# Kernel optimization log

Measured on AMD Instinct MI355X. Metric: run time of the kernel, lower is better.

Reference implementation:

```python
import jax, jax.numpy as jnp
import numpy as np

N_NODES = 100000
N_EDGES = 1600000
IN_DIM, HID, OUT_DIM = 8, 64, 32
LN_EPS = 1e-5


def _layer_norm(x, g, b):
    m = jnp.mean(x, axis=-1, keepdims=True)
    v = jnp.var(x, axis=-1, keepdims=True)
    return g * (x - m) / jnp.sqrt(v + LN_EPS) + b


def _gat(h, W, a, src, dst, n_nodes):
    # Wh: [N, H]
    Wh = h @ W
    # per-edge score: dot(Wh[src], Wh[dst]) * sum(a)  (leaky relu, slope 0.2)
    s = jnp.sum(Wh[src] * Wh[dst], axis=-1)  # [E]
    e = jax.nn.leaky_relu(s * jnp.sum(a), negative_slope=0.2)
    att = jax.nn.softmax(e)  # NOTE: global softmax over ALL edges, as in source
    msg = att[:, None] * Wh[src]  # [E, H]
    h_prime = jax.ops.segment_sum(msg, dst, num_segments=n_nodes)
    return jax.nn.elu(h_prime)


def _stack(x, src, dst, params):
    out = x
    for (W, a, g, b) in params:
        out = _layer_norm(_gat(out, W, a, src, dst, N_NODES), g, b)
    return out


def setup_inputs() -> dict:
    key = jax.random.key(0)
    ks = jax.random.split(key, 24)
    d = {}
    d['x'] = jax.random.normal(ks[0], (N_NODES, IN_DIM), dtype=jnp.float32)
    d['edge_index'] = jax.random.randint(ks[1], (2, N_EDGES), 0, N_NODES, dtype=jnp.int32)
    d['edge_type'] = jax.random.randint(ks[2], (N_EDGES,), 0, 2, dtype=jnp.int32)
    d['temporal_edge_index'] = jax.random.randint(ks[3], (2, N_EDGES), 0, N_NODES, dtype=jnp.int32)

    def xavier(k, shape):
        fan_in, fan_out = shape[0], shape[1]
        lim = float(np.sqrt(6.0 / (fan_in + fan_out)))
        return jax.random.uniform(k, shape, jnp.float32, -lim, lim)

    i = 4
    for pfx in ('s', 't'):
        for li, ind in enumerate((IN_DIM, HID)):
            d[f'{pfx}W{li}'] = xavier(ks[i], (ind, HID)); i += 1
            d[f'{pfx}a{li}'] = xavier(ks[i], (2 * HID, 1)); i += 1
            d[f'{pfx}g{li}'] = jnp.ones((HID,), jnp.float32)
            d[f'{pfx}b{li}'] = jnp.zeros((HID,), jnp.float32)
    d['cW1'] = xavier(ks[i], (HID, OUT_DIM)); i += 1
    d['cb1'] = jnp.zeros((OUT_DIM,), jnp.float32)
    d['cW2'] = xavier(ks[i], (OUT_DIM, 1)); i += 1
    d['cb2'] = jnp.zeros((1,), jnp.float32)
    return d


def reference(x, edge_index, edge_type, temporal_edge_index,
              sW0, sa0, sg0, sb0, sW1, sa1, sg1, sb1,
              tW0, ta0, tg0, tb0, tW1, ta1, tg1, tb1,
              cW1, cb1, cW2, cb2):
    sp = _stack(x, edge_index[0], edge_index[1],
                [(sW0, sa0, sg0, sb0), (sW1, sa1, sg1, sb1)])
    tp = _stack(x, temporal_edge_index[0], temporal_edge_index[1],
                [(tW0, ta0, tg0, tb0), (tW1, ta1, tg1, tb1)])
    h = sp + tp
    h = jax.nn.relu(h @ cW1 + cb1)
    return jax.nn.sigmoid(h @ cW2 + cb2)  # [N, 1]
```

## Files before the change

### kernel.cpp

```cpp
#include <hip/hip_runtime.h>
#include <math.h>

#define NN 100000
#define NE 1600000
#define HID 64
#define NBE 2048
#define EPB 2048
#define NBLK 782
#define NBUCK 98
#define MATN (2 * NBUCK * NBLK)

__device__ __forceinline__ void smerge(float& m, float& z, float m2, float z2) {
    if (m2 > m) { z = z * __expf(m - m2) + z2; m = m2; }
    else if (m2 > -INFINITY) { z += z2 * __expf(m2 - m); }
}

__global__ void prep4(const float* __restrict__ a0, const float* __restrict__ a1,
                      const float* __restrict__ a2, const float* __restrict__ a3,
                      float* __restrict__ sum_a) {
    int w = threadIdx.x >> 6, lane = threadIdx.x & 63;
    const float* a = (w == 0) ? a0 : (w == 1) ? a1 : (w == 2) ? a2 : a3;
    float v = a[lane] + a[lane + 64];
    #pragma unroll
    for (int o = 32; o >= 1; o >>= 1) v += __shfl_xor(v, o);
    if (lane == 0) sum_a[w] = v;
}

__global__ void bucket_hist(const int* __restrict__ eiS, const int* __restrict__ eiT,
                            int* __restrict__ cnt) {
    __shared__ int hist[NBUCK];
    int t = threadIdx.x;
    int side = blockIdx.x >= NBLK;
    int blk = blockIdx.x - side * NBLK;
    const int* dst = (side ? eiT : eiS) + NE;
    if (t < NBUCK) hist[t] = 0;
    __syncthreads();
    int base = blk * EPB;
    #pragma unroll
    for (int k = 0; k < EPB / 256; k++) {
        int e = base + k * 256 + t;
        if (e < NE) atomicAdd(&hist[dst[e] >> 10], 1);
    }
    __syncthreads();
    if (t < NBUCK) cnt[side * (NBUCK * NBLK) + t * NBLK + blk] = hist[t];
}

__global__ void scanA(const int* __restrict__ deg, int* __restrict__ rowtmp,
                      int* __restrict__ bsum, int n) {
    __shared__ int sh[256];
    int t = threadIdx.x;
    int base = blockIdx.x * 1024 + t * 4;
    int a0 = (base + 0 < n) ? deg[base + 0] : 0;
    int a1 = (base + 1 < n) ? deg[base + 1] : 0;
    int a2 = (base + 2 < n) ? deg[base + 2] : 0;
    int a3 = (base + 3 < n) ? deg[base + 3] : 0;
    int s = a0 + a1 + a2 + a3;
    sh[t] = s;
    __syncthreads();
    for (int off = 1; off < 256; off <<= 1) {
        int x = (t >= off) ? sh[t - off] : 0;
        __syncthreads();
        sh[t] += x;
        __syncthreads();
    }
    int excl = sh[t] - s;
    if (t == 255) bsum[blockIdx.x] = sh[255];
    if (base + 0 < n) rowtmp[base + 0] = excl;
    if (base + 1 < n) rowtmp[base + 1] = excl + a0;
    if (base + 2 < n) rowtmp[base + 2] = excl + a0 + a1;
    if (base + 3 < n) rowtmp[base + 3] = excl + a0 + a1 + a2;
}

__global__ void scanB(int* __restrict__ bsum, int nb) {
    __shared__ int sh[256];
    int t = threadIdx.x;
    int v = (t < nb) ? bsum[t] : 0;
    sh[t] = v;
    __syncthreads();
    for (int off = 1; off < 256; off <<= 1) {
        int x = (t >= off) ? sh[t - off] : 0;
        __syncthreads();
        sh[t] += x;
        __syncthreads();
    }
    if (t < nb) bsum[t] = sh[t] - v;
}

__global__ void scanC(const int* __restrict__ rowtmp, const int* __restrict__ bsum,
                      int* __restrict__ outp, int n, int total) {
    int i = blockIdx.x * 256 + threadIdx.x;
    if (i < n) outp[i] = rowtmp[i] + bsum[i >> 10];
    if (i == n) outp[n] = total;
}

__global__ void bucket_scatter(const int* __restrict__ eiS, const int* __restrict__ eiT,
                               const int* __restrict__ off, int2* __restrict__ part) {
    __shared__ int cur[NBUCK];
    int t = threadIdx.x;
    int side = blockIdx.x >= NBLK;
    int blk = blockIdx.x - side * NBLK;
    const int* ei = side ? eiT : eiS;
    if (t < NBUCK) cur[t] = off[side * (NBUCK * NBLK) + t * NBLK + blk];
    __syncthreads();
    int base = blk * EPB;
    #pragma unroll
    for (int k = 0; k < EPB / 256; k++) {
        int e = base + k * 256 + t;
        if (e < NE) {
            int s = ei[e], d = ei[NE + e];
            int p = atomicAdd(&cur[d >> 10], 1);
            part[p] = make_int2(s, d);
        }
    }
}

__global__ void bucket_csr(const int2* __restrict__ part, const int* __restrict__ off,
                           int* __restrict__ rowptrS, int* __restrict__ rowptrT,
                           int* __restrict__ csrsS, int* __restrict__ csrsT) {
    __shared__ int hist[1024];
    __shared__ int sh[1024];
    int t = threadIdx.x;
    int g = blockIdx.x;
    int side = g >= NBUCK;
    int bin = g - side * NBUCK;
    int start = off[g * NBLK];
    int end = off[(g + 1) * NBLK];
    hist[t] = 0;
    __syncthreads();
    for (int i = start + t; i < end; i += 1024)
        atomicAdd(&hist[part[i].y & 1023], 1);
    __syncthreads();
    int own = hist[t];
    sh[t] = own;
    __syncthreads();
    for (int o = 1; o < 1024; o <<= 1) {
        int x = (t >= o) ? sh[t - o] : 0;
        __syncthreads();
        sh[t] += x;
        __syncthreads();
    }
    int excl = sh[t] - own;
    int node = bin * 1024 + t;
    int* rowptr = side ? rowptrT : rowptrS;
    if (node < NN) rowptr[node] = (start - side * NE) + excl;
    if (t == 0 && bin == NBUCK - 1) rowptr[NN] = NE;
    __syncthreads();
    hist[t] = start + excl;
    __syncthreads();
    int* csr = side ? csrsT : csrsS;
    int sub = side * NE;
    for (int i = start + t; i < end; i += 1024) {
        int2 e = part[i];
        int p = atomicAdd(&hist[e.y & 1023], 1);
        csr[p - sub] = e.x;
    }
}

template <int K>
__global__ void gemm_k(const float* __restrict__ h, const float* __restrict__ W,
                       float* __restrict__ Wh, int n) {
    __shared__ float Wl[K][HID];
    int t = threadIdx.x;
    for (int i = t; i < K * HID / 4; i += 256)
        ((float4*)Wl)[i] = ((const float4*)W)[i];
    __syncthreads();
    int node = blockIdx.x * 64 + (t >> 2);
    int c0 = (t & 3) * 16;
    if (node >= n) return;
    float acc[16];
    #pragma unroll
    for (int j = 0; j < 16; j++) acc[j] = 0.f;
    const float* hr = h + (size_t)node * K;
    #pragma unroll
    for (int k4 = 0; k4 < K / 4; k4++) {
        float4 hv = *(const float4*)(hr + k4 * 4);
        #pragma unroll
        for (int j = 0; j < 16; j++)
            acc[j] += hv.x * Wl[k4*4+0][c0+j] + hv.y * Wl[k4*4+1][c0+j]
                    + hv.z * Wl[k4*4+2][c0+j] + hv.w * Wl[k4*4+3][c0+j];
    }
    float* o = Wh + (size_t)node * HID + c0;
    #pragma unroll
    for (int j = 0; j < 16; j += 4)
        *(float4*)(o + j) = make_float4(acc[j], acc[j+1], acc[j+2], acc[j+3]);
}

__global__ void edge_agg(const float* __restrict__ Wh, const int* __restrict__ rowptr,
                         const int* __restrict__ csrs, const float* __restrict__ sum_a_p,
                         float* __restrict__ acc, float* __restrict__ mloc,
                         float* __restrict__ bmax, float* __restrict__ bsumz, int n) {
    int t = threadIdx.x;
    int w = t >> 6, lane = t & 63;
    int g = lane >> 4, l16 = lane & 15;
    float sa = *sum_a_p;
    float M = -INFINITY, Z = 0.f;
    for (int node = blockIdx.x * 4 + w; node < n; node += NBE * 4) {
        float4 q4 = *(const float4*)(Wh + (size_t)node * HID + l16 * 4);
        int beg = rowptr[node], end = rowptr[node + 1];
        float m = -INFINITY, z = 0.f;
        float4 a4 = make_float4(0.f, 0.f, 0.f, 0.f);
        for (int i = beg; i < end; i += 4) {
            int idx = i + g;
            bool act = idx < end;
            int s = csrs[act ? idx : beg];
            float4 v4 = *(const float4*)(Wh + (size_t)s * HID + l16 * 4);
            float x = q4.x*v4.x + q4.y*v4.y + q4.z*v4.z + q4.w*v4.w;
            x += __shfl_xor(x, 1); x += __shfl_xor(x, 2);
            x += __shfl_xor(x, 4); x += __shfl_xor(x, 8);
            float e = x * sa;
            e = e > 0.f ? e : 0.2f * e;
            if (act) {
                if (e > m) {
                    float f = __expf(m - e);
                    z *= f; a4.x *= f; a4.y *= f; a4.z *= f; a4.w *= f;
                    m = e;
                }
                float wgt = __expf(e - m);
                z += wgt;
                a4.x += wgt * v4.x; a4.y += wgt * v4.y;
                a4.z += wgt * v4.z; a4.w += wgt * v4.w;
            }
        }
        #pragma unroll
        for (int o = 16; o <= 32; o <<= 1) {
            float mo = __shfl_xor(m, o), zo = __shfl_xor(z, o);
            float ax = __shfl_xor(a4.x, o), ay = __shfl_xor(a4.y, o);
            float az = __shfl_xor(a4.z, o), aw = __shfl_xor(a4.w, o);
            float mn = fmaxf(m, mo);
            float fs = (m  > -INFINITY) ? __expf(m  - mn) : 0.f;
            float fo = (mo > -INFINITY) ? __expf(mo - mn) : 0.f;
            z = z * fs + zo * fo;
            a4.x = a4.x*fs + ax*fo; a4.y = a4.y*fs + ay*fo;
            a4.z = a4.z*fs + az*fo; a4.w = a4.w*fs + aw*fo;
            m = mn;
        }
        if (g == 0) {
            *(float4*)(acc + (size_t)node * HID + l16 * 4) = a4;
            if (l16 == 0) mloc[node] = m;
        }
        smerge(M, Z, m, z);
    }
    __shared__ float shm[4], shz[4];
    if (lane == 0) { shm[w] = M; shz[w] = Z; }
    __syncthreads();
    if (t == 0) {
        float Mb = shm[0], Zb = shz[0];
        #pragma unroll
        for (int k = 1; k < 4; k++) smerge(Mb, Zb, shm[k], shz[k]);
        bmax[blockIdx.x] = Mb; bsumz[blockIdx.x] = Zb;
    }
}

__global__ void combine_k(const float* __restrict__ bmax, const float* __restrict__ bsumz,
                          float* __restrict__ mz, int nb) {
    int t = threadIdx.x;
    float m = -INFINITY;
    for (int i = t; i < nb; i += 256) m = fmaxf(m, bmax[i]);
    #pragma unroll
    for (int o = 32; o >= 1; o >>= 1) m = fmaxf(m, __shfl_xor(m, o));
    __shared__ float sm[4];
    if ((t & 63) == 0) sm[t >> 6] = m;
    __syncthreads();
    m = fmaxf(fmaxf(sm[0], sm[1]), fmaxf(sm[2], sm[3]));
    double z = 0.0;
    for (int i = t; i < nb; i += 256) {
        float bm = bmax[i];
        if (bm > -INFINITY) z += (double)bsumz[i] * exp((double)bm - (double)m);
    }
    #pragma unroll
    for (int o = 32; o >= 1; o >>= 1) z += __shfl_xor(z, o);
    __shared__ double sz[4];
    if ((t & 63) == 0) sz[t >> 6] = z;
    __syncthreads();
    if (t == 0) { mz[0] = m; mz[1] = (float)(1.0 / (sz[0] + sz[1] + sz[2] + sz[3])); }
}

__global__ void norm_ln(const float* __restrict__ acc, const float* __restrict__ mloc,
                        const float* __restrict__ mz, const float* __restrict__ g,
                        const float* __restrict__ b, float* __restrict__ out, int n) {
    int node = blockIdx.x * 4 + (threadIdx.x >> 6);
    int lane = threadIdx.x & 63;
    if (node >= n) return;
    float scale = __expf(mloc[node] - mz[0]) * mz[1];
    float v = acc[(size_t)node * HID + lane] * scale;
    v = v > 0.f ? v : expm1f(v);
    float s = v, s2 = v * v;
    #pragma unroll
    for (int o = 32; o >= 1; o >>= 1) {
        s += __shfl_xor(s, o);
        s2 += __shfl_xor(s2, o);
    }
    float mean = s * (1.f / 64.f);
    float var = s2 * (1.f / 64.f) - mean * mean;
    out[(size_t)node * HID + lane] = g[lane] * (v - mean) * rsqrtf(var + 1e-5f) + b[lane];
}

__global__ void final_kernel(const float* __restrict__ sp, const float* __restrict__ tp,
                             const float* __restrict__ cW1, const float* __restrict__ cb1,
                             const float* __restrict__ cW2, const float* __restrict__ cb2,
                             float* __restrict__ out, int n) {
    __shared__ float W1[64 * 32];
    __shared__ float W2[32];
    __shared__ float B1[32];
    __shared__ float hsh[8][64];
    int t = threadIdx.x;
    for (int i = t; i < 2048; i += 256) W1[i] = cW1[i];
    if (t < 32) { W2[t] = cW2[t]; B1[t] = cb1[t]; }
    __syncthreads();
    int ln = t >> 5;
    int j = t & 31;
    int node = blockIdx.x * 8 + ln;
    if (node < n) {
        hsh[ln][j]      = sp[(size_t)node * 64 + j]      + tp[(size_t)node * 64 + j];
        hsh[ln][j + 32] = sp[(size_t)node * 64 + j + 32] + tp[(size_t)node * 64 + j + 32];
    }
    __syncthreads();
    if (node >= n) return;
    float a = B1[j];
    #pragma unroll
    for (int k = 0; k < 64; k++) a += hsh[ln][k] * W1[k * 32 + j];
    a = fmaxf(a, 0.f);
    float p = a * W2[j];
    #pragma unroll
    for (int o = 16; o >= 1; o >>= 1) p += __shfl_xor(p, o, 32);
    if (j == 0) out[node] = 1.f / (1.f + expf(-(p + cb2[0])));
}

extern "C" void kernel_launch(void* const* d_in, const int* in_sizes, int n_in,
                              void* d_out, int out_size, void* d_ws, size_t ws_size,
                              hipStream_t stream) {
    const float* x   = (const float*)d_in[0];
    const int*   ei  = (const int*)d_in[1];
    const int*   tei = (const int*)d_in[3];
    const float* sW0 = (const float*)d_in[4],  *sa0 = (const float*)d_in[5];
    const float* sg0 = (const float*)d_in[6],  *sb0 = (const float*)d_in[7];
    const float* sW1 = (const float*)d_in[8],  *sa1 = (const float*)d_in[9];
    const float* sg1 = (const float*)d_in[10], *sb1 = (const float*)d_in[11];
    const float* tW0 = (const float*)d_in[12], *ta0 = (const float*)d_in[13];
    const float* tg0 = (const float*)d_in[14], *tb0 = (const float*)d_in[15];
    const float* tW1 = (const float*)d_in[16], *ta1 = (const float*)d_in[17];
    const float* tg1 = (const float*)d_in[18], *tb1 = (const float*)d_in[19];
    const float* cW1 = (const float*)d_in[20], *cb1 = (const float*)d_in[21];
    const float* cW2 = (const float*)d_in[22], *cb2 = (const float*)d_in[23];
    float* out = (float*)d_out;

    float* ws = (float*)d_ws;
    size_t o = 0;
    float* buf_h  = ws + o; o += (size_t)NN * HID;
    float* buf_Wh = ws + o; o += (size_t)NN * HID;
    float* buf_sp = ws + o; o += (size_t)NN * HID;
    float* mloc   = ws + o; o += NN;
    float* bmax   = ws + o; o += NBE;
    float* bsumz  = ws + o; o += NBE;
    float* sum_a  = ws + o; o += 4;
    float* mz     = ws + o; o += 4;
    int* ip = (int*)(ws + o);
    int* rowptrS = ip; ip += NN + 1;
    int* rowptrT = ip; ip += NN + 1;
    int* csrsS   = ip; ip += NE;
    int* csrsT   = ip; ip += NE;

    int2* part   = (int2*)buf_h;
    int*  cnt    = (int*)buf_Wh;
    int*  offm   = cnt + (MATN + 1);
    int*  rowtmp = offm + (MATN + 1);
    int*  bsum   = rowtmp + MATN;

    const int NSB = (MATN + 1023) / 1024;

    bucket_hist<<<2 * NBLK, 256, 0, stream>>>(ei, tei, cnt);
    scanA<<<NSB, 256, 0, stream>>>(cnt, rowtmp, bsum, MATN);
    scanB<<<1, 256, 0, stream>>>(bsum, NSB);
    scanC<<<(MATN + 256) / 256, 256, 0, stream>>>(rowtmp, bsum, offm, MATN, 2 * NE);
    bucket_scatter<<<2 * NBLK, 256, 0, stream>>>(ei, tei, offm, part);
    bucket_csr<<<2 * NBUCK, 1024, 0, stream>>>(part, offm, rowptrS, rowptrT, csrsS, csrsT);

    prep4<<<1, 256, 0, stream>>>(sa0, sa1, ta0, ta1, sum_a);

    auto run_layer = [&](const float* hin, int K, const float* W, int ai,
                         const float* g, const float* b,
                         const int* rowptr, const int* csrs,
                         float* accb, float* hout) {
        if (K == 8)
            gemm_k<8><<<(NN + 63) / 64, 256, 0, stream>>>(hin, W, buf_Wh, NN);
        else
            gemm_k<64><<<(NN + 63) / 64, 256, 0, stream>>>(hin, W, buf_Wh, NN);
        edge_agg<<<NBE, 256, 0, stream>>>(buf_Wh, rowptr, csrs, sum_a + ai,
                                          accb, mloc, bmax, bsumz, NN);
        combine_k<<<1, 256, 0, stream>>>(bmax, bsumz, mz, NBE);
        norm_ln<<<(NN + 3) / 4, 256, 0, stream>>>(accb, mloc, mz, g, b, hout, NN);
    };

    run_layer(x,     8,  sW0, 0, sg0, sb0, rowptrS, csrsS, buf_h, buf_h);
    run_layer(buf_h, 64, sW1, 1, sg1, sb1, rowptrS, csrsS, buf_h, buf_sp);
    run_layer(x,     8,  tW0, 2, tg0, tb0, rowptrT, csrsT, buf_h, buf_h);
    run_layer(buf_h, 64, tW1, 3, tg1, tb1, rowptrT, csrsT, buf_h, buf_h);

    final_kernel<<<(NN + 7) / 8, 256, 0, stream>>>(buf_sp, buf_h, cW1, cb1, cW2, cb2, out, NN);
}
```

Before: 548.0 us.

## Batch spatial and temporal stacks into shared launches and fuse norm with next GEMM

The spatial and temporal GAT stacks now run together in each launch, split by block index, which halves the number of kernel launches and doubles parallelism per launch. The global softmax combine is folded into the consumer kernels, and layer norm is fused with the next layer's GEMM and with the final MLP, so intermediate h buffers are no longer written and reread. The edge aggregation switches to 8 edges per wave with 8 floats per lane and a branchless online-softmax update. In exchange, every consumer block redundantly recomputes the combine over 2048 partials, and the combine drops from double to float accumulation.

```diff
diff --git a/kernel.cpp b/kernel.cpp
--- a/kernel.cpp
+++ b/kernel.cpp
@@ -5,15 +5,13 @@
 #define NE 1600000
 #define HID 64
 #define NBE 2048
+#define NBG 2048
+#define NBF 2048
 #define EPB 2048
 #define NBLK 782
 #define NBUCK 98
 #define MATN (2 * NBUCK * NBLK)
-
-__device__ __forceinline__ void smerge(float& m, float& z, float m2, float z2) {
-    if (m2 > m) { z = z * __expf(m - m2) + z2; m = m2; }
-    else if (m2 > -INFINITY) { z += z2 * __expf(m2 - m); }
-}
+#define BIGNEG -1.0e30f
 
 __global__ void prep4(const float* __restrict__ a0, const float* __restrict__ a1,
                       const float* __restrict__ a2, const float* __restrict__ a3,
@@ -156,23 +154,28 @@
     }
 }
 
-template <int K>
-__global__ void gemm_k(const float* __restrict__ h, const float* __restrict__ W,
-                       float* __restrict__ Wh, int n) {
-    __shared__ float Wl[K][HID];
-    int t = threadIdx.x;
-    for (int i = t; i < K * HID / 4; i += 256)
+__global__ void gemm2_k8(const float* __restrict__ x, const float* __restrict__ WS,
+                         const float* __restrict__ WT, float* __restrict__ WhS,
+                         float* __restrict__ WhT, int n) {
+    const int nbh = (NN + 63) / 64;
+    int side = blockIdx.x >= nbh;
+    int blk = blockIdx.x - side * nbh;
+    const float* W = side ? WT : WS;
+    float* Wh = side ? WhT : WhS;
+    __shared__ float Wl[8][HID];
+    int t = threadIdx.x;
+    for (int i = t; i < 8 * HID / 4; i += 256)
         ((float4*)Wl)[i] = ((const float4*)W)[i];
     __syncthreads();
-    int node = blockIdx.x * 64 + (t >> 2);
+    int node = blk * 64 + (t >> 2);
     int c0 = (t & 3) * 16;
     if (node >= n) return;
     float acc[16];
     #pragma unroll
     for (int j = 0; j < 16; j++) acc[j] = 0.f;
-    const float* hr = h + (size_t)node * K;
-    #pragma unroll
-    for (int k4 = 0; k4 < K / 4; k4++) {
+    const float* hr = x + (size_t)node * 8;
+    #pragma unroll
+    for (int k4 = 0; k4 < 2; k4++) {
         float4 hv = *(const float4*)(hr + k4 * 4);
         #pragma unroll
         for (int j = 0; j < 16; j++)
@@ -185,60 +188,77 @@
         *(float4*)(o + j) = make_float4(acc[j], acc[j+1], acc[j+2], acc[j+3]);
 }
 
-__global__ void edge_agg(const float* __restrict__ Wh, const int* __restrict__ rowptr,
-                         const int* __restrict__ csrs, const float* __restrict__ sum_a_p,
-                         float* __restrict__ acc, float* __restrict__ mloc,
-                         float* __restrict__ bmax, float* __restrict__ bsumz, int n) {
+__global__ void edge_agg2(const float* __restrict__ WhS, const float* __restrict__ WhT,
+                          const int* __restrict__ rowptrS, const int* __restrict__ rowptrT,
+                          const int* __restrict__ csrsS, const int* __restrict__ csrsT,
+                          const float* __restrict__ sum_a, int aiS, int aiT,
+                          float* __restrict__ accS, float* __restrict__ accT,
+                          float* __restrict__ mlocS, float* __restrict__ mlocT,
+                          float* __restrict__ bmax, float* __restrict__ bsumz, int n) {
+    int side = blockIdx.x >= NBE;
+    int blk = blockIdx.x - side * NBE;
+    const float* Wh = side ? WhT : WhS;
+    const int* rowptr = side ? rowptrT : rowptrS;
+    const int* csrs = side ? csrsT : csrsS;
+    float* acc = side ? accT : accS;
+    float* mloc = side ? mlocT : mlocS;
+    float sa = sum_a[side ? aiT : aiS];
     int t = threadIdx.x;
     int w = t >> 6, lane = t & 63;
-    int g = lane >> 4, l16 = lane & 15;
-    float sa = *sum_a_p;
-    float M = -INFINITY, Z = 0.f;
-    for (int node = blockIdx.x * 4 + w; node < n; node += NBE * 4) {
-        float4 q4 = *(const float4*)(Wh + (size_t)node * HID + l16 * 4);
+    int g = lane >> 3, l8 = lane & 7;
+    float M = BIGNEG, Z = 0.f;
+    for (int node = blk * 4 + w; node < n; node += NBE * 4) {
+        const float* qp = Wh + (size_t)node * HID + l8 * 8;
+        float4 q0 = *(const float4*)qp, q1 = *(const float4*)(qp + 4);
         int beg = rowptr[node], end = rowptr[node + 1];
-        float m = -INFINITY, z = 0.f;
-        float4 a4 = make_float4(0.f, 0.f, 0.f, 0.f);
-        for (int i = beg; i < end; i += 4) {
+        float m = BIGNEG, z = 0.f;
+        float4 a0 = make_float4(0,0,0,0), a1 = make_float4(0,0,0,0);
+        for (int i = beg; i < end; i += 8) {
             int idx = i + g;
             bool act = idx < end;
             int s = csrs[act ? idx : beg];
-            float4 v4 = *(const float4*)(Wh + (size_t)s * HID + l16 * 4);
-            float x = q4.x*v4.x + q4.y*v4.y + q4.z*v4.z + q4.w*v4.w;
-            x += __shfl_xor(x, 1); x += __shfl_xor(x, 2);
-            x += __shfl_xor(x, 4); x += __shfl_xor(x, 8);
+            const float* vp = Wh + (size_t)s * HID + l8 * 8;
+            float4 v0 = *(const float4*)vp, v1 = *(const float4*)(vp + 4);
+            float x = q0.x*v0.x + q0.y*v0.y + q0.z*v0.z + q0.w*v0.w
+                    + q1.x*v1.x + q1.y*v1.y + q1.z*v1.z + q1.w*v1.w;
+            x += __shfl_xor(x, 1); x += __shfl_xor(x, 2); x += __shfl_xor(x, 4);
             float e = x * sa;
             e = e > 0.f ? e : 0.2f * e;
-            if (act) {
-                if (e > m) {
-                    float f = __expf(m - e);
-                    z *= f; a4.x *= f; a4.y *= f; a4.z *= f; a4.w *= f;
-                    m = e;
-                }
-                float wgt = __expf(e - m);
-                z += wgt;
-                a4.x += wgt * v4.x; a4.y += wgt * v4.y;
-                a4.z += wgt * v4.z; a4.w += wgt * v4.w;
-            }
-        }
-        #pragma unroll
-        for (int o = 16; o <= 32; o <<= 1) {
+            e = act ? e : BIGNEG;
+            float mn = fmaxf(m, e);
+            float fs = __expf(m - mn);
+            float wg = act ? __expf(e - mn) : 0.f;
+            z = z * fs + wg;
+            a0.x = a0.x*fs + wg*v0.x; a0.y = a0.y*fs + wg*v0.y;
+            a0.z = a0.z*fs + wg*v0.z; a0.w = a0.w*fs + wg*v0.w;
+            a1.x = a1.x*fs + wg*v1.x; a1.y = a1.y*fs + wg*v1.y;
+            a1.z = a1.z*fs + wg*v1.z; a1.w = a1.w*fs + wg*v1.w;
+            m = mn;
+        }
+        #pragma unroll
+        for (int o = 8; o <= 32; o <<= 1) {
             float mo = __shfl_xor(m, o), zo = __shfl_xor(z, o);
-            float ax = __shfl_xor(a4.x, o), ay = __shfl_xor(a4.y, o);
-            float az = __shfl_xor(a4.z, o), aw = __shfl_xor(a4.w, o);
+            float b0x = __shfl_xor(a0.x, o), b0y = __shfl_xor(a0.y, o);
+            float b0z = __shfl_xor(a0.z, o), b0w = __shfl_xor(a0.w, o);
+            float b1x = __shfl_xor(a1.x, o), b1y = __shfl_xor(a1.y, o);
+            float b1z = __shfl_xor(a1.z, o), b1w = __shfl_xor(a1.w, o);
             float mn = fmaxf(m, mo);
-            float fs = (m  > -INFINITY) ? __expf(m  - mn) : 0.f;
-            float fo = (mo > -INFINITY) ? __expf(mo - mn) : 0.f;
+            float fs = __expf(m - mn), fo = __expf(mo - mn);
             z = z * fs + zo * fo;
-            a4.x = a4.x*fs + ax*fo; a4.y = a4.y*fs + ay*fo;
-            a4.z = a4.z*fs + az*fo; a4.w = a4.w*fs + aw*fo;
+            a0.x = a0.x*fs + b0x*fo; a0.y = a0.y*fs + b0y*fo;
+            a0.z = a0.z*fs + b0z*fo; a0.w = a0.w*fs + b0w*fo;
+            a1.x = a1.x*fs + b1x*fo; a1.y = a1.y*fs + b1y*fo;
+            a1.z = a1.z*fs + b1z*fo; a1.w = a1.w*fs + b1w*fo;
             m = mn;
         }
         if (g == 0) {
-            *(float4*)(acc + (size_t)node * HID + l16 * 4) = a4;
-            if (l16 == 0) mloc[node] = m;
-        }
-        smerge(M, Z, m, z);
+            float* ap = acc + (size_t)node * HID + l8 * 8;
+            *(float4*)ap = a0; *(float4*)(ap + 4) = a1;
+            if (l8 == 0) mloc[node] = m;
+        }
+        float mn2 = fmaxf(M, m);
+        Z = Z * __expf(M - mn2) + z * __expf(m - mn2);
+        M = mn2;
     }
     __shared__ float shm[4], shz[4];
     if (lane == 0) { shm[w] = M; shz[w] = Z; }
@@ -246,84 +266,136 @@
     if (t == 0) {
         float Mb = shm[0], Zb = shz[0];
         #pragma unroll
-        for (int k = 1; k < 4; k++) smerge(Mb, Zb, shm[k], shz[k]);
+        for (int k = 1; k < 4; k++) {
+            float mn = fmaxf(Mb, shm[k]);
+            Zb = Zb * __expf(Mb - mn) + shz[k] * __expf(shm[k] - mn);
+            Mb = mn;
+        }
         bmax[blockIdx.x] = Mb; bsumz[blockIdx.x] = Zb;
     }
 }
 
-__global__ void combine_k(const float* __restrict__ bmax, const float* __restrict__ bsumz,
-                          float* __restrict__ mz, int nb) {
-    int t = threadIdx.x;
-    float m = -INFINITY;
-    for (int i = t; i < nb; i += 256) m = fmaxf(m, bmax[i]);
-    #pragma unroll
-    for (int o = 32; o >= 1; o >>= 1) m = fmaxf(m, __shfl_xor(m, o));
-    __shared__ float sm[4];
-    if ((t & 63) == 0) sm[t >> 6] = m;
-    __syncthreads();
-    m = fmaxf(fmaxf(sm[0], sm[1]), fmaxf(sm[2], sm[3]));
-    double z = 0.0;
-    for (int i = t; i < nb; i += 256) {
-        float bm = bmax[i];
-        if (bm > -INFINITY) z += (double)bsumz[i] * exp((double)bm - (double)m);
-    }
-    #pragma unroll
-    for (int o = 32; o >= 1; o >>= 1) z += __shfl_xor(z, o);
-    __shared__ double sz[4];
-    if ((t & 63) == 0) sz[t >> 6] = z;
-    __syncthreads();
-    if (t == 0) { mz[0] = m; mz[1] = (float)(1.0 / (sz[0] + sz[1] + sz[2] + sz[3])); }
-}
-
-__global__ void norm_ln(const float* __restrict__ acc, const float* __restrict__ mloc,
-                        const float* __restrict__ mz, const float* __restrict__ g,
-                        const float* __restrict__ b, float* __restrict__ out, int n) {
-    int node = blockIdx.x * 4 + (threadIdx.x >> 6);
-    int lane = threadIdx.x & 63;
-    if (node >= n) return;
-    float scale = __expf(mloc[node] - mz[0]) * mz[1];
-    float v = acc[(size_t)node * HID + lane] * scale;
-    v = v > 0.f ? v : expm1f(v);
-    float s = v, s2 = v * v;
-    #pragma unroll
-    for (int o = 32; o >= 1; o >>= 1) {
-        s += __shfl_xor(s, o);
-        s2 += __shfl_xor(s2, o);
-    }
-    float mean = s * (1.f / 64.f);
-    float var = s2 * (1.f / 64.f) - mean * mean;
-    out[(size_t)node * HID + lane] = g[lane] * (v - mean) * rsqrtf(var + 1e-5f) + b[lane];
-}
-
-__global__ void final_kernel(const float* __restrict__ sp, const float* __restrict__ tp,
-                             const float* __restrict__ cW1, const float* __restrict__ cb1,
-                             const float* __restrict__ cW2, const float* __restrict__ cb2,
-                             float* __restrict__ out, int n) {
-    __shared__ float W1[64 * 32];
-    __shared__ float W2[32];
-    __shared__ float B1[32];
-    __shared__ float hsh[8][64];
-    int t = threadIdx.x;
-    for (int i = t; i < 2048; i += 256) W1[i] = cW1[i];
-    if (t < 32) { W2[t] = cW2[t]; B1[t] = cb1[t]; }
-    __syncthreads();
-    int ln = t >> 5;
-    int j = t & 31;
-    int node = blockIdx.x * 8 + ln;
-    if (node < n) {
-        hsh[ln][j]      = sp[(size_t)node * 64 + j]      + tp[(size_t)node * 64 + j];
-        hsh[ln][j + 32] = sp[(size_t)node * 64 + j + 32] + tp[(size_t)node * 64 + j + 32];
-    }
-    __syncthreads();
-    if (node >= n) return;
-    float a = B1[j];
-    #pragma unroll
-    for (int k = 0; k < 64; k++) a += hsh[ln][k] * W1[k * 32 + j];
-    a = fmaxf(a, 0.f);
-    float p = a * W2[j];
-    #pragma unroll
-    for (int o = 16; o >= 1; o >>= 1) p += __shfl_xor(p, o, 32);
-    if (j == 0) out[node] = 1.f / (1.f + expf(-(p + cb2[0])));
+__device__ __forceinline__ void combine_side(const float* __restrict__ bmax,
+                                             const float* __restrict__ bsumz,
+                                             int base, float* shred, float& gm, float& invZ) {
+    int t = threadIdx.x;
+    float lm = BIGNEG;
+    for (int i = t; i < NBE; i += 256) lm = fmaxf(lm, bmax[base + i]);
+    #pragma unroll
+    for (int o = 32; o >= 1; o >>= 1) lm = fmaxf(lm, __shfl_xor(lm, o));
+    if ((t & 63) == 0) shred[t >> 6] = lm;
+    __syncthreads();
+    float m = fmaxf(fmaxf(shred[0], shred[1]), fmaxf(shred[2], shred[3]));
+    __syncthreads();
+    float lz = 0.f;
+    for (int i = t; i < NBE; i += 256) lz += bsumz[base + i] * __expf(bmax[base + i] - m);
+    #pragma unroll
+    for (int o = 32; o >= 1; o >>= 1) lz += __shfl_xor(lz, o);
+    if ((t & 63) == 0) shred[t >> 6] = lz;
+    __syncthreads();
+    float Zt = (shred[0] + shred[1]) + (shred[2] + shred[3]);
+    __syncthreads();
+    gm = m; invZ = 1.f / Zt;
+}
+
+__global__ void normgemm2(const float* __restrict__ accS, const float* __restrict__ accT,
+                          const float* __restrict__ mlocS, const float* __restrict__ mlocT,
+                          const float* __restrict__ bmax, const float* __restrict__ bsumz,
+                          const float* __restrict__ gS, const float* __restrict__ bS,
+                          const float* __restrict__ gT, const float* __restrict__ bT,
+                          const float* __restrict__ W1S, const float* __restrict__ W1T,
+                          float* __restrict__ WhS, float* __restrict__ WhT, int n) {
+    int side = blockIdx.x >= NBG;
+    int blk = blockIdx.x - side * NBG;
+    const float* acc = side ? accT : accS;
+    const float* mloc = side ? mlocT : mlocS;
+    const float* g = side ? gT : gS;
+    const float* b = side ? bT : bS;
+    const float* W1 = side ? W1T : W1S;
+    float* Wh = side ? WhT : WhS;
+    __shared__ float shred[4];
+    float gm, invZ;
+    combine_side(bmax, bsumz, side * NBE, shred, gm, invZ);
+    __shared__ float Wl[64 * 64];
+    int t = threadIdx.x;
+    for (int i = t; i < 1024; i += 256)
+        ((float4*)Wl)[i] = ((const float4*)W1)[i];
+    __syncthreads();
+    __shared__ float hrow[4][64];
+    int w = t >> 6, lane = t & 63;
+    float gl = g[lane], bl = b[lane];
+    for (int node = blk * 4 + w; node < n; node += NBG * 4) {
+        float scale = __expf(mloc[node] - gm) * invZ;
+        float v = acc[(size_t)node * HID + lane] * scale;
+        v = v > 0.f ? v : expm1f(v);
+        float s = v, s2 = v * v;
+        #pragma unroll
+        for (int o = 32; o >= 1; o >>= 1) {
+            s += __shfl_xor(s, o);
+            s2 += __shfl_xor(s2, o);
+        }
+        float mean = s * (1.f / 64.f);
+        float var = s2 * (1.f / 64.f) - mean * mean;
+        float hn = gl * (v - mean) * rsqrtf(var + 1e-5f) + bl;
+        hrow[w][lane] = hn;
+        float o2 = 0.f;
+        #pragma unroll
+        for (int k = 0; k < 64; k++) o2 += hrow[w][k] * Wl[k * 64 + lane];
+        Wh[(size_t)node * HID + lane] = o2;
+    }
+}
+
+__global__ void normfinal(const float* __restrict__ accS, const float* __restrict__ accT,
+                          const float* __restrict__ mlocS, const float* __restrict__ mlocT,
+                          const float* __restrict__ bmax, const float* __restrict__ bsumz,
+                          const float* __restrict__ gS, const float* __restrict__ bS,
+                          const float* __restrict__ gT, const float* __restrict__ bT,
+                          const float* __restrict__ cW1, const float* __restrict__ cb1,
+                          const float* __restrict__ cW2, const float* __restrict__ cb2,
+                          float* __restrict__ out, int n) {
+    __shared__ float shred[4];
+    float gmS, invZS, gmT, invZT;
+    combine_side(bmax, bsumz, 0, shred, gmS, invZS);
+    combine_side(bmax, bsumz, NBE, shred, gmT, invZT);
+    __shared__ float W1l[64 * 32];
+    __shared__ float W2l[32], B1l[32];
+    int t = threadIdx.x;
+    for (int i = t; i < 512; i += 256)
+        ((float4*)W1l)[i] = ((const float4*)cW1)[i];
+    if (t < 32) { W2l[t] = cW2[t]; B1l[t] = cb1[t]; }
+    __syncthreads();
+    float c2 = cb2[0];
+    __shared__ float hrow[4][64];
+    int w = t >> 6, lane = t & 63;
+    int j = lane & 31;
+    float glS = gS[lane], blS = bS[lane], glT = gT[lane], blT = bT[lane];
+    for (int node = blockIdx.x * 4 + w; node < n; node += NBF * 4) {
+        float vS = accS[(size_t)node * HID + lane] * (__expf(mlocS[node] - gmS) * invZS);
+        vS = vS > 0.f ? vS : expm1f(vS);
+        float sA = vS, sB = vS * vS;
+        #pragma unroll
+        for (int o = 32; o >= 1; o >>= 1) { sA += __shfl_xor(sA, o); sB += __shfl_xor(sB, o); }
+        float meanS = sA * (1.f / 64.f);
+        float varS = sB * (1.f / 64.f) - meanS * meanS;
+        float hS = glS * (vS - meanS) * rsqrtf(varS + 1e-5f) + blS;
+        float vT = accT[(size_t)node * HID + lane] * (__expf(mlocT[node] - gmT) * invZT);
+        vT = vT > 0.f ? vT : expm1f(vT);
+        sA = vT; sB = vT * vT;
+        #pragma unroll
+        for (int o = 32; o >= 1; o >>= 1) { sA += __shfl_xor(sA, o); sB += __shfl_xor(sB, o); }
+        float meanT = sA * (1.f / 64.f);
+        float varT = sB * (1.f / 64.f) - meanT * meanT;
+        float hT = glT * (vT - meanT) * rsqrtf(varT + 1e-5f) + blT;
+        hrow[w][lane] = hS + hT;
+        float a = B1l[j];
+        #pragma unroll
+        for (int k = 0; k < 64; k++) a += hrow[w][k] * W1l[k * 32 + j];
+        a = fmaxf(a, 0.f);
+        float p = a * W2l[j];
+        #pragma unroll
+        for (int o = 16; o >= 1; o >>= 1) p += __shfl_xor(p, o, 32);
+        if (lane == 0) out[node] = 1.f / (1.f + expf(-(p + c2)));
+    }
 }
 
 extern "C" void kernel_launch(void* const* d_in, const int* in_sizes, int n_in,
@@ -346,22 +418,23 @@
 
     float* ws = (float*)d_ws;
     size_t o = 0;
-    float* buf_h  = ws + o; o += (size_t)NN * HID;
-    float* buf_Wh = ws + o; o += (size_t)NN * HID;
-    float* buf_sp = ws + o; o += (size_t)NN * HID;
-    float* mloc   = ws + o; o += NN;
-    float* bmax   = ws + o; o += NBE;
-    float* bsumz  = ws + o; o += NBE;
-    float* sum_a  = ws + o; o += 4;
-    float* mz     = ws + o; o += 4;
+    float* hS  = ws + o; o += (size_t)NN * HID;
+    float* hT  = ws + o; o += (size_t)NN * HID;
+    float* WhS = ws + o; o += (size_t)NN * HID;
+    float* WhT = ws + o; o += (size_t)NN * HID;
+    float* mlocS = ws + o; o += NN;
+    float* mlocT = ws + o; o += NN;
+    float* bmax  = ws + o; o += 2 * NBE;
+    float* bsumz = ws + o; o += 2 * NBE;
+    float* sum_a = ws + o; o += 4;
     int* ip = (int*)(ws + o);
     int* rowptrS = ip; ip += NN + 1;
     int* rowptrT = ip; ip += NN + 1;
     int* csrsS   = ip; ip += NE;
     int* csrsT   = ip; ip += NE;
 
-    int2* part   = (int2*)buf_h;
-    int*  cnt    = (int*)buf_Wh;
+    int2* part   = (int2*)WhS;
+    int*  cnt    = (int*)WhT;
     int*  offm   = cnt + (MATN + 1);
     int*  rowtmp = offm + (MATN + 1);
     int*  bsum   = rowtmp + MATN;
@@ -377,24 +450,17 @@
 
     prep4<<<1, 256, 0, stream>>>(sa0, sa1, ta0, ta1, sum_a);
 
-    auto run_layer = [&](const float* hin, int K, const float* W, int ai,
-                         const float* g, const float* b,
-                         const int* rowptr, const int* csrs,
-                         float* accb, float* hout) {
-        if (K == 8)
-            gemm_k<8><<<(NN + 63) / 64, 256, 0, stream>>>(hin, W, buf_Wh, NN);
-        else
-            gemm_k<64><<<(NN + 63) / 64, 256, 0, stream>>>(hin, W, buf_Wh, NN);
-        edge_agg<<<NBE, 256, 0, stream>>>(buf_Wh, rowptr, csrs, sum_a + ai,
-                                          accb, mloc, bmax, bsumz, NN);
-        combine_k<<<1, 256, 0, stream>>>(bmax, bsumz, mz, NBE);
-        norm_ln<<<(NN + 3) / 4, 256, 0, stream>>>(accb, mloc, mz, g, b, hout, NN);
-    };
-
-    run_layer(x,     8,  sW0, 0, sg0, sb0, rowptrS, csrsS, buf_h, buf_h);
-    run_layer(buf_h, 64, sW1, 1, sg1, sb1, rowptrS, csrsS, buf_h, buf_sp);
-    run_layer(x,     8,  tW0, 2, tg0, tb0, rowptrT, csrsT, buf_h, buf_h);
-    run_layer(buf_h, 64, tW1, 3, tg1, tb1, rowptrT, csrsT, buf_h, buf_h);
-
-    final_kernel<<<(NN + 7) / 8, 256, 0, stream>>>(buf_sp, buf_h, cW1, cb1, cW2, cb2, out, NN);
-}
+    const int nbh = (NN + 63) / 64;
+
+    gemm2_k8<<<2 * nbh, 256, 0, stream>>>(x, sW0, tW0, WhS, WhT, NN);
+    edge_agg2<<<2 * NBE, 256, 0, stream>>>(WhS, WhT, rowptrS, rowptrT, csrsS, csrsT,
+                                           sum_a, 0, 2, hS, hT, mlocS, mlocT,
+                                           bmax, bsumz, NN);
+    normgemm2<<<2 * NBG, 256, 0, stream>>>(hS, hT, mlocS, mlocT, bmax, bsumz,
+                                           sg0, sb0, tg0, tb0, sW1, tW1, WhS, WhT, NN);
+    edge_agg2<<<2 * NBE, 256, 0, stream>>>(WhS, WhT, rowptrS, rowptrT, csrsS, csrsT,
+                                           sum_a, 1, 3, hS, hT, mlocS, mlocT,
+                                           bmax, bsumz, NN);
+    normfinal<<<NBF, 256, 0, stream>>>(hS, hT, mlocS, mlocT, bmax, bsumz,
+                                       sg1, sb1, tg1, tb1, cW1, cb1, cW2, cb2, out, NN);
+}
```

After: 492.1 us. 10.2% less time.
